# Performance work log

Measured on AMD Instinct MI355X. Metric: run time of the kernel, lower is better.

Reference implementation:

```python
import jax, jax.numpy as jnp
import numpy as np

DIM = 1024
B, T = 4, 8192


def setup_inputs() -> dict:
    key = jax.random.key(0)
    ks = jax.random.split(key, 5)
    scale = 1.0 / np.sqrt(DIM)
    x = jax.random.normal(ks[0], (B, T, DIM), dtype=jnp.float32)
    w_in = jax.random.uniform(ks[1], (DIM, DIM), jnp.float32, -scale, scale)
    b_in = jax.random.uniform(ks[2], (DIM,), jnp.float32, -scale, scale)
    a = jnp.zeros((DIM,), jnp.float32)   # nn.Parameter(torch.zeros(dim))
    b = jnp.ones((DIM,), jnp.float32)    # nn.Parameter(torch.ones(dim))
    w_out = jax.random.uniform(ks[3], (DIM, DIM), jnp.float32, -scale, scale)
    b_out = jax.random.uniform(ks[4], (DIM,), jnp.float32, -scale, scale)
    return {"x": x, "w_in": w_in, "b_in": b_in, "a": a, "b": b,
            "w_out": w_out, "b_out": b_out}


def reference(x, w_in, b_in, a, b, w_out, b_out):
    # h = in_proj(x): [B, T, D]
    h = jnp.einsum('btd,ed->bte', x, w_in) + b_in
    A = jax.nn.sigmoid(a)  # [D], diagonal transition

    def step(state, h_t):
        state = A * state + b * h_t  # [B, D]
        return state, state

    init = jnp.zeros_like(h[:, 0])  # [B, D]
    _, ys = jax.lax.scan(step, init, jnp.swapaxes(h, 0, 1))  # ys: [T, B, D]
    y = jnp.swapaxes(ys, 0, 1)  # [B, T, D]
    return jnp.einsum('btd,ed->bte', y, w_out) + b_out
```

## Files before the change

kernel.cpp:

```cpp
#include <hip/hip_runtime.h>
#include <hip/hip_bf16.h>
#include <cstdint>

#define DIM 1024
#define BATCH 4
#define SEQ 8192
#define M_TOTAL (BATCH * SEQ)

#define CH 64
#define CL (SEQ / CH)

using bf16 = __hip_bfloat16;
typedef __attribute__((ext_vector_type(4))) float f32x4;
typedef __attribute__((ext_vector_type(8))) __bf16 bf16x8;

__global__ void convert_all(const float* __restrict__ x, bf16* __restrict__ xb,
                            const float* __restrict__ w1, bf16* __restrict__ w1b,
                            const float* __restrict__ w2, bf16* __restrict__ w2b,
                            long n4x, long n4w) {
    long i = blockIdx.x * (long)blockDim.x + threadIdx.x;
    const float* in;
    bf16* out;
    long off;
    if (i < n4x)              { in = x;  out = xb;  off = i; }
    else if (i < n4x + n4w)   { in = w1; out = w1b; off = i - n4x; }
    else if (i < n4x + 2*n4w) { in = w2; out = w2b; off = i - n4x - n4w; }
    else return;
    const float4 v = ((const float4*)in)[off];
    __hip_bfloat162* o = (__hip_bfloat162*)(out + off * 4);
    o[0] = __float22bfloat162_rn(make_float2(v.x, v.y));
    o[1] = __float22bfloat162_rn(make_float2(v.z, v.w));
}

template <int OUT_MODE>
__global__ __launch_bounds__(256) void gemm_bt_kernel(
    const bf16* __restrict__ A, const bf16* __restrict__ B,
    const float* __restrict__ bias, void* __restrict__ C,
    int M, int N, int K) {
    __shared__ __align__(16) char lds[2 * 128 * 64 * 2];
    char* ldsA = lds;
    char* ldsB = lds + 128 * 64 * 2;

    const int tid  = threadIdx.x;
    const int wave = tid >> 6;
    const int lane = tid & 63;
    const int bn = blockIdx.x;
    const int bm = blockIdx.y;
    const int wm = (wave >> 1) * 64;
    const int wn = (wave & 1) * 64;

    f32x4 acc[4][4];
#pragma unroll
    for (int i = 0; i < 4; i++)
#pragma unroll
        for (int j = 0; j < 4; j++) acc[i][j] = (f32x4){0.f, 0.f, 0.f, 0.f};

    const long arow_base = (long)bm * 128;
    const long brow_base = (long)bn * 128;

    const int fr_row = lane & 15;
    const int fr_kb  = lane >> 4;

    for (int k0 = 0; k0 < K; k0 += 64) {
#pragma unroll
        for (int r = 0; r < 4; r++) {
            int c = tid + r * 256;
            int row = c >> 3;
            int kc = (c & 7) ^ (row & 7);
            const bf16* ga = A + (arow_base + row) * (long)K + k0 + kc * 8;
            const bf16* gb = B + (brow_base + row) * (long)K + k0 + kc * 8;
            __builtin_amdgcn_global_load_lds(
                (const __attribute__((address_space(1))) void*)ga,
                (__attribute__((address_space(3))) void*)(ldsA + c * 16),
                16, 0, 0);
            __builtin_amdgcn_global_load_lds(
                (const __attribute__((address_space(1))) void*)gb,
                (__attribute__((address_space(3))) void*)(ldsB + c * 16),
                16, 0, 0);
        }
        __syncthreads();

#pragma unroll
        for (int ks = 0; ks < 2; ks++) {
            bf16x8 af[4], bfg[4];
#pragma unroll
            for (int i = 0; i < 4; i++) {
                int row = wm + i * 16 + fr_row;
                int cc = ks * 4 + fr_kb;
                int chunk = row * 8 + (cc ^ (row & 7));
                af[i] = *(const bf16x8*)(ldsA + chunk * 16);
            }
#pragma unroll
            for (int j = 0; j < 4; j++) {
                int row = wn + j * 16 + fr_row;
                int cc = ks * 4 + fr_kb;
                int chunk = row * 8 + (cc ^ (row & 7));
                bfg[j] = *(const bf16x8*)(ldsB + chunk * 16);
            }
#pragma unroll
            for (int i = 0; i < 4; i++)
#pragma unroll
                for (int j = 0; j < 4; j++)
                    acc[i][j] = __builtin_amdgcn_mfma_f32_16x16x32_bf16(
                        af[i], bfg[j], acc[i][j], 0, 0, 0);
        }
        __syncthreads();
    }

    const int crow = (lane >> 4) * 4;
    const int ccol = lane & 15;
#pragma unroll
    for (int i = 0; i < 4; i++) {
#pragma unroll
        for (int j = 0; j < 4; j++) {
            long mbase = (long)bm * 128 + wm + i * 16 + crow;
            int n = bn * 128 + wn + j * 16 + ccol;
            float bv = bias[n];
#pragma unroll
            for (int r = 0; r < 4; r++) {
                float v = acc[i][j][r] + bv;
                long idx = (mbase + r) * (long)N + n;
                if (OUT_MODE == 0)
                    ((bf16*)C)[idx] = __float2bfloat16(v);
                else
                    ((float*)C)[idx] = v;
            }
        }
    }
}

__global__ __launch_bounds__(1024) void scan_pass1(
    const bf16* __restrict__ h, const float* __restrict__ a,
    const float* __restrict__ bcoef, float* __restrict__ S) {
    const int d = threadIdx.x;
    const int blk = blockIdx.x;
    const int b = blk / CH, c = blk % CH;
    const float Ad = 1.f / (1.f + expf(-a[d]));
    const float bd = bcoef[d];
    float s = 0.f;
    const bf16* hp = h + ((long)b * SEQ + (long)c * CL) * DIM + d;
#pragma unroll 8
    for (int t = 0; t < CL; t++)
        s = Ad * s + bd * __bfloat162float(hp[(long)t * DIM]);
    S[((long)b * CH + c) * DIM + d] = s;
}

__global__ __launch_bounds__(1024) void scan_pass3(
    bf16* __restrict__ h, const float* __restrict__ a,
    const float* __restrict__ bcoef, const float* __restrict__ S) {
    const int d = threadIdx.x;
    const int blk = blockIdx.x;
    const int b = blk / CH, c = blk % CH;
    const float Ad = 1.f / (1.f + expf(-a[d]));
    const float bd = bcoef[d];
    float Ap = Ad;
#pragma unroll
    for (int i = 0; i < 7; i++) Ap *= Ap;

    float carry = 0.f;
    const float* Sp = S + (long)b * CH * DIM + d;
    for (int i0 = 0; i0 < c; i0 += 8) {
        float sv[8];
        int nn = (c - i0 < 8) ? (c - i0) : 8;
#pragma unroll 8
        for (int j = 0; j < 8; j++)
            if (j < nn) sv[j] = Sp[(long)(i0 + j) * DIM];
#pragma unroll 8
        for (int j = 0; j < 8; j++)
            if (j < nn) carry = Ap * carry + sv[j];
    }

    float s = carry;
    bf16* hp = h + ((long)b * SEQ + (long)c * CL) * DIM + d;
#pragma unroll 8
    for (int t = 0; t < CL; t++) {
        s = Ad * s + bd * __bfloat162float(hp[(long)t * DIM]);
        hp[(long)t * DIM] = __float2bfloat16(s);
    }
}

extern "C" void kernel_launch(void* const* d_in, const int* in_sizes, int n_in,
                              void* d_out, int out_size, void* d_ws,
                              size_t ws_size, hipStream_t stream) {
    const float* x     = (const float*)d_in[0];
    const float* w_in  = (const float*)d_in[1];
    const float* b_in  = (const float*)d_in[2];
    const float* a     = (const float*)d_in[3];
    const float* bcoef = (const float*)d_in[4];
    const float* w_out = (const float*)d_in[5];
    const float* b_out = (const float*)d_in[6];
    float* out = (float*)d_out;

    char* ws = (char*)d_ws;
    bf16* xb  = (bf16*)ws;  ws += (size_t)M_TOTAL * DIM * 2;
    bf16* wib = (bf16*)ws;  ws += (size_t)DIM * DIM * 2;
    bf16* wob = (bf16*)ws;  ws += (size_t)DIM * DIM * 2;
    bf16* h   = (bf16*)ws;  ws += (size_t)M_TOTAL * DIM * 2;
    float* S  = (float*)ws; ws += (size_t)BATCH * CH * DIM * 4;

    {
        long n4x = (long)M_TOTAL * DIM / 4;
        long n4w = (long)DIM * DIM / 4;
        long total = n4x + 2 * n4w;
        convert_all<<<(int)((total + 255) / 256), 256, 0, stream>>>(
            x, xb, w_in, wib, w_out, wob, n4x, n4w);
    }

    dim3 gg(DIM / 128, M_TOTAL / 128);

    gemm_bt_kernel<0><<<gg, 256, 0, stream>>>(xb, wib, b_in, h, M_TOTAL, DIM, DIM);

    scan_pass1<<<BATCH * CH, DIM, 0, stream>>>(h, a, bcoef, S);
    scan_pass3<<<BATCH * CH, DIM, 0, stream>>>(h, a, bcoef, S);

    gemm_bt_kernel<1><<<gg, 256, 0, stream>>>(h, wob, b_out, out, M_TOTAL, DIM, DIM);
}
```

Measured before the change: 448.8 us.

## Use 32x32 MFMA, XCD-aware block swizzle, and bf16x2 vectorized scans

```diff
diff --git a/kernel.cpp b/kernel.cpp
--- a/kernel.cpp
+++ b/kernel.cpp
@@ -11,7 +11,7 @@
 #define CL (SEQ / CH)
 
 using bf16 = __hip_bfloat16;
-typedef __attribute__((ext_vector_type(4))) float f32x4;
+typedef __attribute__((ext_vector_type(16))) float f32x16;
 typedef __attribute__((ext_vector_type(8))) __bf16 bf16x8;
 
 __global__ void convert_all(const float* __restrict__ x, bf16* __restrict__ xb,
@@ -44,22 +44,29 @@
     const int tid  = threadIdx.x;
     const int wave = tid >> 6;
     const int lane = tid & 63;
-    const int bn = blockIdx.x;
-    const int bm = blockIdx.y;
+
+    const int L   = blockIdx.x;
+    const int xcd = L & 7;
+    const int li  = L >> 3;
+    const int bm  = xcd * 32 + (li >> 3);
+    const int bn  = li & 7;
+
     const int wm = (wave >> 1) * 64;
     const int wn = (wave & 1) * 64;
 
-    f32x4 acc[4][4];
-#pragma unroll
-    for (int i = 0; i < 4; i++)
-#pragma unroll
-        for (int j = 0; j < 4; j++) acc[i][j] = (f32x4){0.f, 0.f, 0.f, 0.f};
+    f32x16 acc[2][2];
+#pragma unroll
+    for (int i = 0; i < 2; i++)
+#pragma unroll
+        for (int j = 0; j < 2; j++)
+#pragma unroll
+            for (int r = 0; r < 16; r++) acc[i][j][r] = 0.f;
 
     const long arow_base = (long)bm * 128;
     const long brow_base = (long)bn * 128;
 
-    const int fr_row = lane & 15;
-    const int fr_kb  = lane >> 4;
+    const int r31   = lane & 31;
+    const int khalf = lane >> 5;
 
     for (int k0 = 0; k0 < K; k0 += 64) {
 #pragma unroll
@@ -81,45 +88,45 @@
         __syncthreads();
 
 #pragma unroll
-        for (int ks = 0; ks < 2; ks++) {
-            bf16x8 af[4], bfg[4];
-#pragma unroll
-            for (int i = 0; i < 4; i++) {
-                int row = wm + i * 16 + fr_row;
-                int cc = ks * 4 + fr_kb;
-                int chunk = row * 8 + (cc ^ (row & 7));
+        for (int s = 0; s < 4; s++) {
+            const int kc = s * 2 + khalf;
+            bf16x8 af[2], bfv[2];
+#pragma unroll
+            for (int i = 0; i < 2; i++) {
+                int row = wm + i * 32 + r31;
+                int chunk = row * 8 + (kc ^ (row & 7));
                 af[i] = *(const bf16x8*)(ldsA + chunk * 16);
             }
 #pragma unroll
-            for (int j = 0; j < 4; j++) {
-                int row = wn + j * 16 + fr_row;
-                int cc = ks * 4 + fr_kb;
-                int chunk = row * 8 + (cc ^ (row & 7));
-                bfg[j] = *(const bf16x8*)(ldsB + chunk * 16);
+            for (int j = 0; j < 2; j++) {
+                int row = wn + j * 32 + r31;
+                int chunk = row * 8 + (kc ^ (row & 7));
+                bfv[j] = *(const bf16x8*)(ldsB + chunk * 16);
             }
 #pragma unroll
-            for (int i = 0; i < 4; i++)
-#pragma unroll
-                for (int j = 0; j < 4; j++)
-                    acc[i][j] = __builtin_amdgcn_mfma_f32_16x16x32_bf16(
-                        af[i], bfg[j], acc[i][j], 0, 0, 0);
+            for (int i = 0; i < 2; i++)
+#pragma unroll
+                for (int j = 0; j < 2; j++)
+                    acc[i][j] = __builtin_amdgcn_mfma_f32_32x32x16_bf16(
+                        af[i], bfv[j], acc[i][j], 0, 0, 0);
         }
         __syncthreads();
     }
 
-    const int crow = (lane >> 4) * 4;
-    const int ccol = lane & 15;
-#pragma unroll
-    for (int i = 0; i < 4; i++) {
-#pragma unroll
-        for (int j = 0; j < 4; j++) {
-            long mbase = (long)bm * 128 + wm + i * 16 + crow;
-            int n = bn * 128 + wn + j * 16 + ccol;
+    const int ccol  = lane & 31;
+    const int rbase = 4 * (lane >> 5);
+#pragma unroll
+    for (int i = 0; i < 2; i++) {
+#pragma unroll
+        for (int j = 0; j < 2; j++) {
+            int n = bn * 128 + wn + j * 32 + ccol;
             float bv = bias[n];
 #pragma unroll
-            for (int r = 0; r < 4; r++) {
+            for (int r = 0; r < 16; r++) {
+                int rowt = (r & 3) + 8 * (r >> 2) + rbase;
+                long m = (long)bm * 128 + wm + i * 32 + rowt;
                 float v = acc[i][j][r] + bv;
-                long idx = (mbase + r) * (long)N + n;
+                long idx = m * (long)N + n;
                 if (OUT_MODE == 0)
                     ((bf16*)C)[idx] = __float2bfloat16(v);
                 else
@@ -129,53 +136,65 @@
     }
 }
 
-__global__ __launch_bounds__(1024) void scan_pass1(
+__global__ __launch_bounds__(512) void scan_pass1(
     const bf16* __restrict__ h, const float* __restrict__ a,
     const float* __restrict__ bcoef, float* __restrict__ S) {
-    const int d = threadIdx.x;
+    const int d2 = threadIdx.x;
     const int blk = blockIdx.x;
     const int b = blk / CH, c = blk % CH;
-    const float Ad = 1.f / (1.f + expf(-a[d]));
-    const float bd = bcoef[d];
-    float s = 0.f;
-    const bf16* hp = h + ((long)b * SEQ + (long)c * CL) * DIM + d;
-#pragma unroll 8
-    for (int t = 0; t < CL; t++)
-        s = Ad * s + bd * __bfloat162float(hp[(long)t * DIM]);
-    S[((long)b * CH + c) * DIM + d] = s;
-}
-
-__global__ __launch_bounds__(1024) void scan_pass3(
+    const float A0 = 1.f / (1.f + expf(-a[2 * d2]));
+    const float A1 = 1.f / (1.f + expf(-a[2 * d2 + 1]));
+    const float b0 = bcoef[2 * d2];
+    const float b1 = bcoef[2 * d2 + 1];
+    float s0 = 0.f, s1 = 0.f;
+    const __hip_bfloat162* hp =
+        (const __hip_bfloat162*)(h + ((long)b * SEQ + (long)c * CL) * DIM) + d2;
+#pragma unroll 8
+    for (int t = 0; t < CL; t++) {
+        float2 v = __bfloat1622float2(hp[(long)t * (DIM / 2)]);
+        s0 = A0 * s0 + b0 * v.x;
+        s1 = A1 * s1 + b1 * v.y;
+    }
+    float2* Sp = (float2*)(S + ((long)b * CH + c) * DIM) + d2;
+    *Sp = make_float2(s0, s1);
+}
+
+__global__ __launch_bounds__(512) void scan_pass3(
     bf16* __restrict__ h, const float* __restrict__ a,
     const float* __restrict__ bcoef, const float* __restrict__ S) {
-    const int d = threadIdx.x;
+    const int d2 = threadIdx.x;
     const int blk = blockIdx.x;
     const int b = blk / CH, c = blk % CH;
-    const float Ad = 1.f / (1.f + expf(-a[d]));
-    const float bd = bcoef[d];
-    float Ap = Ad;
-#pragma unroll
-    for (int i = 0; i < 7; i++) Ap *= Ap;
-
-    float carry = 0.f;
-    const float* Sp = S + (long)b * CH * DIM + d;
+    const float A0 = 1.f / (1.f + expf(-a[2 * d2]));
+    const float A1 = 1.f / (1.f + expf(-a[2 * d2 + 1]));
+    const float b0 = bcoef[2 * d2];
+    const float b1 = bcoef[2 * d2 + 1];
+    float Ap0 = A0, Ap1 = A1;
+#pragma unroll
+    for (int i = 0; i < 7; i++) { Ap0 *= Ap0; Ap1 *= Ap1; }
+
+    float c0 = 0.f, c1 = 0.f;
+    const float2* Sp = (const float2*)(S + (long)b * CH * DIM) + d2;
     for (int i0 = 0; i0 < c; i0 += 8) {
-        float sv[8];
+        float2 sv[8];
         int nn = (c - i0 < 8) ? (c - i0) : 8;
 #pragma unroll 8
         for (int j = 0; j < 8; j++)
-            if (j < nn) sv[j] = Sp[(long)(i0 + j) * DIM];
+            if (j < nn) sv[j] = Sp[(long)(i0 + j) * (DIM / 2)];
 #pragma unroll 8
         for (int j = 0; j < 8; j++)
-            if (j < nn) carry = Ap * carry + sv[j];
-    }
-
-    float s = carry;
-    bf16* hp = h + ((long)b * SEQ + (long)c * CL) * DIM + d;
+            if (j < nn) { c0 = Ap0 * c0 + sv[j].x; c1 = Ap1 * c1 + sv[j].y; }
+    }
+
+    float s0 = c0, s1 = c1;
+    __hip_bfloat162* hp =
+        (__hip_bfloat162*)(h + ((long)b * SEQ + (long)c * CL) * DIM) + d2;
 #pragma unroll 8
     for (int t = 0; t < CL; t++) {
-        s = Ad * s + bd * __bfloat162float(hp[(long)t * DIM]);
-        hp[(long)t * DIM] = __float2bfloat16(s);
+        float2 v = __bfloat1622float2(hp[(long)t * (DIM / 2)]);
+        s0 = A0 * s0 + b0 * v.x;
+        s1 = A1 * s1 + b1 * v.y;
+        hp[(long)t * (DIM / 2)] = __float22bfloat162_rn(make_float2(s0, s1));
     }
 }
 
@@ -206,12 +225,14 @@
             x, xb, w_in, wib, w_out, wob, n4x, n4w);
     }
 
-    dim3 gg(DIM / 128, M_TOTAL / 128);
-
-    gemm_bt_kernel<0><<<gg, 256, 0, stream>>>(xb, wib, b_in, h, M_TOTAL, DIM, DIM);
-
-    scan_pass1<<<BATCH * CH, DIM, 0, stream>>>(h, a, bcoef, S);
-    scan_pass3<<<BATCH * CH, DIM, 0, stream>>>(h, a, bcoef, S);
-
-    gemm_bt_kernel<1><<<gg, 256, 0, stream>>>(h, wob, b_out, out, M_TOTAL, DIM, DIM);
-}
+    const int nblocks = (M_TOTAL / 128) * (DIM / 128);
+
+    gemm_bt_kernel<0><<<nblocks, 256, 0, stream>>>(xb, wib, b_in, h,
+                                                   M_TOTAL, DIM, DIM);
+
+    scan_pass1<<<BATCH * CH, 512, 0, stream>>>(h, a, bcoef, S);
+    scan_pass3<<<BATCH * CH, 512, 0, stream>>>(h, a, bcoef, S);
+
+    gemm_bt_kernel<1><<<nblocks, 256, 0, stream>>>(h, wob, b_out, out,
+                                                   M_TOTAL, DIM, DIM);
+}
```

Result: faster. 413.0 us (-8.0%).
